# Kernel tuning notes

Measured on AMD Instinct MI355X. Metric: run time of the kernel, lower is better.

## Reference

```python
import jax, jax.numpy as jnp
import numpy as np

FP8_MAX = 448.0  # max normal for float8_e4m3fn
BLOCK = 128


def setup_inputs() -> dict:
    key = jax.random.key(0)
    k1, k2, k3 = jax.random.split(key, 3)
    B, S, D_IN, D_OUT = 2, 2048, 4096, 8192
    x = jax.random.normal(k1, (B, S, D_IN), dtype=jnp.float32)
    # stored weight is fp8_e4m3fn; materialize as f32 values that are exactly fp8-representable
    w = jax.random.normal(k2, (D_OUT, D_IN), dtype=jnp.float32)
    weight = w.astype(jnp.float8_e4m3fn).astype(jnp.float32)
    # positive per-(128x128)-block dequant scales
    weight_scale_inv = (
        jax.random.uniform(k3, (D_OUT // BLOCK, D_IN // BLOCK), dtype=jnp.float32) * 0.05 + 0.005
    )
    return {"x": x, "weight": weight, "weight_scale_inv": weight_scale_inv}


def _quantize_per_token(x2d):
    # x2d: [M, K] -> fp8 values + [M, 1] f32 scale
    amax = jnp.clip(jnp.max(jnp.abs(x2d), axis=-1, keepdims=True), min=1e-12)
    x_scale = (amax / FP8_MAX).astype(jnp.float32)
    x_fp8 = (x2d / x_scale).astype(jnp.float8_e4m3fn)
    return x_fp8, x_scale


def _dequantize_weight(weight, weight_scale_inv):
    # weight: [O, K] (fp8-representable f32), scales: [O/B, K/B]
    O, K = weight.shape
    w_fp8 = weight.astype(jnp.float8_e4m3fn).astype(jnp.float32)
    wb = w_fp8.reshape(O // BLOCK, BLOCK, K // BLOCK, BLOCK)
    wb = wb * weight_scale_inv[:, None, :, None]
    return wb.reshape(O, K)


def reference(x, weight, weight_scale_inv):
    orig_shape = x.shape
    x2d = x.reshape(-1, orig_shape[-1])  # [M, K], M > 1 path
    x_fp8, x_scale = _quantize_per_token(x2d)
    # block-scaled fp8 GEMM: y[m,n] = x_scale[m] * sum_k x_fp8[m,k] * w_fp8[n,k] * s[n//B,k//B]
    w_deq = _dequantize_weight(weight, weight_scale_inv)  # [O, K]
    y = jnp.einsum("mk,ok->mo", x_fp8.astype(jnp.float32), w_deq) * x_scale
    return y.reshape(*orig_shape[:-1], weight.shape[0])
```

## Files before the change

### kernel.cpp

```cpp
#include <hip/hip_runtime.h>

typedef float f32x4  __attribute__((ext_vector_type(4)));
typedef float f32x16 __attribute__((ext_vector_type(16)));
typedef int   i32x4  __attribute__((ext_vector_type(4)));
typedef int   i32x8  __attribute__((ext_vector_type(8)));

#define AS1 __attribute__((address_space(1)))
#define AS3 __attribute__((address_space(3)))

__global__ __launch_bounds__(256) void quant_x_fp8_kernel(
    const float* __restrict__ x, unsigned char* __restrict__ x8,
    float* __restrict__ xs, int K) {
  int m = blockIdx.x;
  int t = threadIdx.x;
  const f32x4* src = (const f32x4*)(x + (size_t)m * K + t * 16);
  f32x4 v[4];
  float am = 0.0f;
#pragma unroll
  for (int i = 0; i < 4; ++i) {
    v[i] = src[i];
#pragma unroll
    for (int j = 0; j < 4; ++j) am = fmaxf(am, __builtin_fabsf(v[i][j]));
  }
#pragma unroll
  for (int off = 32; off >= 1; off >>= 1)
    am = fmaxf(am, __shfl_xor(am, off, 64));
  __shared__ float red[4];
  int wv = t >> 6, lane = t & 63;
  if (lane == 0) red[wv] = am;
  __syncthreads();
  am = fmaxf(fmaxf(red[0], red[1]), fmaxf(red[2], red[3]));
  am = fmaxf(am, 1e-12f);
  float sc = am / 448.0f;
  if (t == 0) xs[m] = sc;
  i32x4 out;
#pragma unroll
  for (int i = 0; i < 4; ++i) {
    float q0 = v[i][0] / sc, q1 = v[i][1] / sc;
    float q2 = v[i][2] / sc, q3 = v[i][3] / sc;
    int p = __builtin_amdgcn_cvt_pk_fp8_f32(q0, q1, 0, false);
    p = __builtin_amdgcn_cvt_pk_fp8_f32(q2, q3, p, true);
    out[i] = p;
  }
  *(i32x4*)(x8 + (size_t)m * K + t * 16) = out;
}

__global__ __launch_bounds__(256) void quant_w_fp8_kernel(
    const float* __restrict__ w, unsigned char* __restrict__ w8) {
  size_t idx = (size_t)blockIdx.x * 256 + threadIdx.x;
  const f32x4* src = (const f32x4*)w + idx * 4;
  i32x4 out;
#pragma unroll
  for (int i = 0; i < 4; ++i) {
    f32x4 v = src[i];
    int p = __builtin_amdgcn_cvt_pk_fp8_f32(v[0], v[1], 0, false);
    p = __builtin_amdgcn_cvt_pk_fp8_f32(v[2], v[3], p, true);
    out[i] = p;
  }
  ((i32x4*)w8)[idx] = out;
}

__global__ __launch_bounds__(512, 1) void gemm_mxfp8_kernel(
    const unsigned char* __restrict__ A8,
    const unsigned char* __restrict__ W8,
    const float* __restrict__ xs,
    const float* __restrict__ wsinv,
    float* __restrict__ Y,
    int M, int N, int K) {
  const int KB = K >> 7;

  int bid = blockIdx.x, nwg = gridDim.x;
  int wg = (bid & 7) * (nwg >> 3) + (bid >> 3);
  int mt = M >> 8;
  int bm = wg & (mt - 1);
  int bn = wg / mt;
  int m0 = bm << 8, n0 = bn << 7;

  __shared__ __align__(16) char lds[147456];

  const int tid = threadIdx.x, wv = tid >> 6, lane = tid & 63;
  const int wr = wv >> 1, wc = wv & 1;
  const int l31 = lane & 31, hi2 = lane >> 5;
  const int salt = l31 & 7;

  const int sL0 = ((hi2 * 2 + 0) ^ salt) << 4;
  const int sH0 = ((hi2 * 2 + 1) ^ salt) << 4;
  const int sL1 = ((4 + hi2 * 2 + 0) ^ salt) << 4;
  const int sH1 = ((4 + hi2 * 2 + 1) ^ salt) << 4;

  const int aRow = (wr * 64 + l31) * 128;
  const int bRow = (wc * 64 + l31) * 128;
  const int aL0 = aRow + sL0, aH0 = aRow + sH0;
  const int aL1 = aRow + sL1, aH1 = aRow + sH1;
  const int bL0 = bRow + sL0, bH0 = bRow + sH0;
  const int bL1 = bRow + sL1, bH1 = bRow + sH1;

  const int stgD = tid << 4;
  const int rIdx = tid >> 3;
  const int cSrc = ((tid & 7) ^ ((tid >> 3) & 7)) << 4;
  const size_t rowB = (size_t)K;
  const size_t g64 = 64 * rowB;
  const char* pA = (const char*)A8 + (size_t)(m0 + rIdx) * rowB + cSrc;
  const char* pB = (const char*)W8 + (size_t)(n0 + rIdx) * rowB + cSrc;

  const float* wsv = wsinv + (size_t)bn * KB;

  f32x16 acc[2][2];
#pragma unroll
  for (int i = 0; i < 2; ++i)
#pragma unroll
    for (int j = 0; j < 2; ++j) acc[i][j] = (f32x16)0.0f;

  i32x8 af[2], bf[2][2];

#define GL(SRC, DST)                                                           \
  __builtin_amdgcn_global_load_lds((const AS1 void*)(SRC), (AS3 void*)(DST),   \
                                   16, 0, 0)
#define STG_A(COND, SB, SRC)                                                   \
  if (COND) {                                                                  \
    const char* s_ = (SRC);                                                    \
    char* d_ = lds + (SB) + stgD;                                              \
    GL(s_, d_);                                                                \
    GL(s_ + g64, d_ + 8192);                                                   \
    GL(s_ + 2 * g64, d_ + 16384);                                              \
    GL(s_ + 3 * g64, d_ + 24576);                                              \
  }
#define STG_B(COND, SB, SRC)                                                   \
  if (COND) {                                                                  \
    const char* s_ = (SRC);                                                    \
    char* d_ = lds + (SB) + stgD;                                              \
    GL(s_, d_);                                                                \
    GL(s_ + g64, d_ + 8192);                                                   \
  }

#define RD_A(RB, MJ)                                                           \
  {                                                                            \
    const char* p_ = lds + (RB) + (MJ) * 4096;                                 \
    i32x4 lo0 = *(const i32x4*)(p_ + aL0);                                     \
    i32x4 hi0 = *(const i32x4*)(p_ + aH0);                                     \
    i32x4 lo1 = *(const i32x4*)(p_ + aL1);                                     \
    i32x4 hi1 = *(const i32x4*)(p_ + aH1);                                     \
    af[0] = __builtin_shufflevector(lo0, hi0, 0, 1, 2, 3, 4, 5, 6, 7);         \
    af[1] = __builtin_shufflevector(lo1, hi1, 0, 1, 2, 3, 4, 5, 6, 7);         \
  }
#define RD_B(RB)                                                               \
  _Pragma("unroll") for (int nj = 0; nj < 2; ++nj) {                           \
    const char* p_ = lds + (RB) + nj * 4096;                                   \
    i32x4 lo0 = *(const i32x4*)(p_ + bL0);                                     \
    i32x4 hi0 = *(const i32x4*)(p_ + bH0);                                     \
    i32x4 lo1 = *(const i32x4*)(p_ + bL1);                                     \
    i32x4 hi1 = *(const i32x4*)(p_ + bH1);                                     \
    bf[nj][0] = __builtin_shufflevector(lo0, hi0, 0, 1, 2, 3, 4, 5, 6, 7);     \
    bf[nj][1] = __builtin_shufflevector(lo1, hi1, 0, 1, 2, 3, 4, 5, 6, 7);     \
  }

#define MMF(MJ, SV)                                                            \
  _Pragma("unroll") for (int nj = 0; nj < 2; ++nj) {                           \
    f32x16 t_ = __builtin_amdgcn_mfma_scale_f32_32x32x64_f8f6f4(               \
        af[0], bf[nj][0], (f32x16)0.0f, 0, 0, 0, 0x7f7f7f7f, 0, 0x7f7f7f7f);   \
    t_ = __builtin_amdgcn_mfma_scale_f32_32x32x64_f8f6f4(                      \
        af[1], bf[nj][1], t_, 0, 0, 0, 0x7f7f7f7f, 0, 0x7f7f7f7f);             \
    _Pragma("unroll") for (int q = 0; q < 16; ++q)                             \
        acc[MJ][nj][q] = __builtin_fmaf(SV, t_[q], acc[MJ][nj][q]);            \
  }

  STG_A(true, 0, pA);
  STG_B(true, 98304, pB);
  STG_A(true, 32768, pA + 128);
  STG_B(true, 114688, pB + 128);
  asm volatile("s_waitcnt vmcnt(6)" ::: "memory");
  __builtin_amdgcn_s_barrier();

  int rdA = 0;
  int stA = 65536;
  int rdB = 98304;
  int stB = 131072;
  const char* pAs = pA + 256;
  const char* pBs = pB + 256;

#define TILE(T, G, VM)                                                         \
  {                                                                            \
    float s_ = wsv[(T)];                                                       \
    RD_B(rdB);                                                                 \
    RD_A(rdA, 0);                                                              \
    STG_A(G, stA, pAs);                                                        \
    STG_B(G, stB, pBs);                                                        \
    __builtin_amdgcn_s_setprio(1);                                             \
    MMF(0, s_);                                                                \
    __builtin_amdgcn_s_setprio(0);                                             \
    RD_A(rdA, 1);                                                              \
    __builtin_amdgcn_s_setprio(1);                                             \
    MMF(1, s_);                                                                \
    __builtin_amdgcn_s_setprio(0);                                             \
    asm volatile("s_waitcnt " VM ::: "memory");                                \
    __builtin_amdgcn_s_barrier();                                              \
    rdA = (rdA == 65536) ? 0 : rdA + 32768;                                    \
    stA = (stA == 65536) ? 0 : stA + 32768;                                    \
    rdB = (rdB == 131072) ? 98304 : rdB + 16384;                               \
    stB = (stB == 131072) ? 98304 : stB + 16384;                               \
    pAs += 128;                                                                \
    pBs += 128;                                                                \
  }

#pragma unroll 1
  for (int t = 0; t < KB - 2; ++t) {
    TILE(t, true, "vmcnt(6)")
  }
  TILE(KB - 2, false, "vmcnt(0)")
  TILE(KB - 1, false, "vmcnt(0)")

#undef TILE
#undef MMF
#undef RD_B
#undef RD_A
#undef STG_B
#undef STG_A
#undef GL

#pragma unroll
  for (int mj = 0; mj < 2; ++mj)
#pragma unroll
    for (int nj = 0; nj < 2; ++nj) {
      int col = n0 + wc * 64 + nj * 32 + l31;
#pragma unroll
      for (int q = 0; q < 4; ++q) {
        int row0 = m0 + wr * 64 + mj * 32 + q * 8 + hi2 * 4;
        f32x4 sv = *(const f32x4*)(xs + row0);
#pragma unroll
        for (int j = 0; j < 4; ++j)
          Y[(size_t)(row0 + j) * N + col] = acc[mj][nj][q * 4 + j] * sv[j];
      }
    }
}

extern "C" void kernel_launch(void* const* d_in, const int* in_sizes, int n_in,
                              void* d_out, int out_size, void* d_ws, size_t ws_size,
                              hipStream_t stream) {
  const float* x     = (const float*)d_in[0];
  const float* w     = (const float*)d_in[1];
  const float* wsinv = (const float*)d_in[2];
  float* y = (float*)d_out;

  const int K = 4096;
  const int M = in_sizes[0] / K;
  const int N = in_sizes[1] / K;

  unsigned char* x8 = (unsigned char*)d_ws;
  float* xs = (float*)((char*)d_ws + (size_t)M * K);
  unsigned char* w8 =
      (unsigned char*)d_ws + (size_t)M * K + (size_t)M * 4;

  quant_x_fp8_kernel<<<M, 256, 0, stream>>>(x, x8, xs, K);
  quant_w_fp8_kernel<<<(int)(((size_t)N * K / 16 + 255) / 256), 256, 0,
                       stream>>>(w, w8);

  dim3 grid((M / 256) * (N / 128));
  gemm_mxfp8_kernel<<<grid, 512, 0, stream>>>(x8, w8, xs, wsinv, y, M, N, K);
}
```

Baseline: 230.6 us.

## Accumulate MFMA directly into accumulators with running scale-ratio rescaling

Instead of running each pair of MFMAs into a zero-initialized temporary and then FMA-ing it into the accumulator with the block scale, the accumulator is multiplied by the ratio of the previous to the current block scale and the MFMAs accumulate into it directly. The last scale is applied once in the epilogue. This removes the temporary accumulator registers and the serial FMA chain after each MFMA pair. It also interleaves the B-fragment LDS reads and the MFMAs per column fragment, with global staging placed between them. It adds a per-tile division and a rescale multiply, and the repeated ratio rescaling can cause small floating-point drift.

```diff
diff --git a/kernel.cpp b/kernel.cpp
--- a/kernel.cpp
+++ b/kernel.cpp
@@ -143,25 +143,25 @@
     af[0] = __builtin_shufflevector(lo0, hi0, 0, 1, 2, 3, 4, 5, 6, 7);         \
     af[1] = __builtin_shufflevector(lo1, hi1, 0, 1, 2, 3, 4, 5, 6, 7);         \
   }
-#define RD_B(RB)                                                               \
-  _Pragma("unroll") for (int nj = 0; nj < 2; ++nj) {                           \
-    const char* p_ = lds + (RB) + nj * 4096;                                   \
+#define RD_Bn(RB, NJ)                                                          \
+  {                                                                            \
+    const char* p_ = lds + (RB) + (NJ) * 4096;                                 \
     i32x4 lo0 = *(const i32x4*)(p_ + bL0);                                     \
     i32x4 hi0 = *(const i32x4*)(p_ + bH0);                                     \
     i32x4 lo1 = *(const i32x4*)(p_ + bL1);                                     \
     i32x4 hi1 = *(const i32x4*)(p_ + bH1);                                     \
-    bf[nj][0] = __builtin_shufflevector(lo0, hi0, 0, 1, 2, 3, 4, 5, 6, 7);     \
-    bf[nj][1] = __builtin_shufflevector(lo1, hi1, 0, 1, 2, 3, 4, 5, 6, 7);     \
-  }
-
-#define MMF(MJ, SV)                                                            \
-  _Pragma("unroll") for (int nj = 0; nj < 2; ++nj) {                           \
-    f32x16 t_ = __builtin_amdgcn_mfma_scale_f32_32x32x64_f8f6f4(               \
-        af[0], bf[nj][0], (f32x16)0.0f, 0, 0, 0, 0x7f7f7f7f, 0, 0x7f7f7f7f);   \
-    t_ = __builtin_amdgcn_mfma_scale_f32_32x32x64_f8f6f4(                      \
-        af[1], bf[nj][1], t_, 0, 0, 0, 0x7f7f7f7f, 0, 0x7f7f7f7f);             \
+    bf[NJ][0] = __builtin_shufflevector(lo0, hi0, 0, 1, 2, 3, 4, 5, 6, 7);     \
+    bf[NJ][1] = __builtin_shufflevector(lo1, hi1, 0, 1, 2, 3, 4, 5, 6, 7);     \
+  }
+
+#define MMFn(MJ, NJ, R_)                                                       \
+  {                                                                            \
     _Pragma("unroll") for (int q = 0; q < 16; ++q)                             \
-        acc[MJ][nj][q] = __builtin_fmaf(SV, t_[q], acc[MJ][nj][q]);            \
+        acc[MJ][NJ][q] *= (R_);                                                \
+    acc[MJ][NJ] = __builtin_amdgcn_mfma_scale_f32_32x32x64_f8f6f4(             \
+        af[0], bf[NJ][0], acc[MJ][NJ], 0, 0, 0, 0x7f7f7f7f, 0, 0x7f7f7f7f);    \
+    acc[MJ][NJ] = __builtin_amdgcn_mfma_scale_f32_32x32x64_f8f6f4(             \
+        af[1], bf[NJ][1], acc[MJ][NJ], 0, 0, 0, 0x7f7f7f7f, 0, 0x7f7f7f7f);    \
   }
 
   STG_A(true, 0, pA);
@@ -177,21 +177,29 @@
   int stB = 131072;
   const char* pAs = pA + 256;
   const char* pBs = pB + 256;
+  float sp_ = wsv[0];
 
 #define TILE(T, G, VM)                                                         \
   {                                                                            \
-    float s_ = wsv[(T)];                                                       \
-    RD_B(rdB);                                                                 \
+    float sc_ = wsv[(T)];                                                      \
+    float r_ = sp_ / sc_;                                                      \
     RD_A(rdA, 0);                                                              \
+    RD_Bn(rdB, 0);                                                             \
+    __builtin_amdgcn_s_setprio(1);                                             \
+    MMFn(0, 0, r_);                                                            \
+    __builtin_amdgcn_s_setprio(0);                                             \
     STG_A(G, stA, pAs);                                                        \
     STG_B(G, stB, pBs);                                                        \
+    RD_Bn(rdB, 1);                                                             \
     __builtin_amdgcn_s_setprio(1);                                             \
-    MMF(0, s_);                                                                \
+    MMFn(0, 1, r_);                                                            \
     __builtin_amdgcn_s_setprio(0);                                             \
     RD_A(rdA, 1);                                                              \
     __builtin_amdgcn_s_setprio(1);                                             \
-    MMF(1, s_);                                                                \
+    MMFn(1, 0, r_);                                                            \
+    MMFn(1, 1, r_);                                                            \
     __builtin_amdgcn_s_setprio(0);                                             \
+    sp_ = sc_;                                                                 \
     asm volatile("s_waitcnt " VM ::: "memory");                                \
     __builtin_amdgcn_s_barrier();                                              \
     rdA = (rdA == 65536) ? 0 : rdA + 32768;                                    \
@@ -210,13 +218,14 @@
   TILE(KB - 1, false, "vmcnt(0)")
 
 #undef TILE
-#undef MMF
-#undef RD_B
+#undef MMFn
+#undef RD_Bn
 #undef RD_A
 #undef STG_B
 #undef STG_A
 #undef GL
 
+  const float sl_ = sp_;
 #pragma unroll
   for (int mj = 0; mj < 2; ++mj)
 #pragma unroll
@@ -228,7 +237,7 @@
         f32x4 sv = *(const f32x4*)(xs + row0);
 #pragma unroll
         for (int j = 0; j < 4; ++j)
-          Y[(size_t)(row0 + j) * N + col] = acc[mj][nj][q * 4 + j] * sv[j];
+          Y[(size_t)(row0 + j) * N + col] = acc[mj][nj][q * 4 + j] * sv[j] * sl_;
       }
     }
 }
```

New measurement: 226.7 us. Within noise of the previous version (-1.7%).
